# Performance work log

Measured on AMD Instinct MI355X. Metric: run time of the kernel, lower is better.

Reference implementation:

```python
import jax, jax.numpy as jnp
import numpy as np


def setup_inputs() -> dict:
    key = jax.random.key(0)
    ks = jax.random.split(key, 6)
    n_sess, n_trials = 4096, 2048
    chose_left = jax.random.bernoulli(ks[0], 0.5, (n_sess, n_trials)).astype(jnp.float32)
    chose_right = 1.0 - chose_left
    outcome = jax.random.bernoulli(ks[1], 0.5, (n_sess, n_trials)).astype(jnp.float32)
    inp = jnp.stack([chose_left, chose_right, outcome], axis=-1)  # (B, T, 3)
    return {
        "input": inp,
        # raw (pre-sigmoid) alpha logits, as stored by torch parametrize
        "a_same_rew": jax.random.normal(ks[2], (1,), jnp.float32),
        "a_same_unrew": jax.random.normal(ks[3], (1,), jnp.float32),
        "a_diff_rew": jax.random.normal(ks[4], (1,), jnp.float32),
        "a_diff_unrew": jax.random.normal(ks[5], (1,), jnp.float32),
        "k_same_rew": jnp.ones((1,), jnp.float32),
        "k_same_unrew": jnp.zeros((1,), jnp.float32),
        "k_diff_rew": jnp.ones((1,), jnp.float32),
        "k_diff_unrew": jnp.zeros((1,), jnp.float32),
    }


def _qvalue_scan(inp, a_sr, a_su, a_dr, a_du, k_sr, k_su, k_dr, k_du):
    # alphas via UnitConstraint (sigmoid of raw logit)
    alphas = jax.nn.sigmoid(jnp.concatenate([a_sr, a_su, a_dr, a_du]))  # (4,)
    ksr, ksu, kdr, kdu = k_sr[0], k_su[0], k_dr[0], k_du[0]
    B = inp.shape[0]

    def step(v, x_t):  # v: (B,2), x_t: (B,3)
        cl, cr, o = x_t[:, 0], x_t[:, 1], x_t[:, 2]
        no = 1.0 - o

        def side(same, other, vcol):
            d = jnp.stack([same * o * (ksr - vcol),
                           same * no * (ksu - vcol),
                           other * o * (kdr - vcol),
                           other * no * (kdu - vcol)], axis=1)  # (B,4)
            return d.sum(axis=1), d @ alphas  # diff, delta per side

        diff_l, del_l = side(cl, cr, v[:, 0])
        diff_r, del_r = side(cr, cl, v[:, 1])
        delta = jnp.stack([del_l, del_r], axis=1)  # (B,2)
        diff = jnp.stack([diff_l, diff_r], axis=1)
        new_v = v + delta
        return new_v, (new_v, diff, delta)

    v0 = jnp.zeros((B, 2), inp.dtype)
    _, (out_v, out_diff, out_delta) = jax.lax.scan(step, v0, jnp.swapaxes(inp, 0, 1))
    # (T,B,2) -> (B,T,2)
    tr = lambda a: jnp.swapaxes(a, 0, 1)
    return tr(out_v), tr(out_diff), tr(out_delta)


def reference(input, a_same_rew, a_same_unrew, a_diff_rew, a_diff_unrew,
              k_same_rew, k_same_unrew, k_diff_rew, k_diff_unrew):
    return _qvalue_scan(input, a_same_rew, a_same_unrew, a_diff_rew, a_diff_unrew,
                        k_same_rew, k_same_unrew, k_diff_rew, k_diff_unrew)
```

## Files before the change

kernel.cpp:

```cpp
#include <hip/hip_runtime.h>
#include <math.h>

#define B_SESS 4096
#define T_TR   2048
#define NCH    256
#define CL     8


__global__ __launch_bounds__(256, 4) void qvalue_kernel(
    const float* __restrict__ inp,
    const float* __restrict__ p_asr, const float* __restrict__ p_asu,
    const float* __restrict__ p_adr, const float* __restrict__ p_adu,
    const float* __restrict__ p_ksr, const float* __restrict__ p_ksu,
    const float* __restrict__ p_kdr, const float* __restrict__ p_kdu,
    float* __restrict__ out)
{
    __shared__ float sIn[T_TR * 3];
    __shared__ float sWT[4 * 4];

    const int s    = blockIdx.x;
    const int tid  = threadIdx.x;
    const int lane = tid & 63;
    const int w    = tid >> 6;

    const float4* in4 = (const float4*)(inp + (size_t)s * (T_TR * 3));
    #pragma unroll
    for (int k = 0; k < 6; ++k) {
        int p4 = k * 256 + tid;
        float4 wv = in4[p4];
        float vals[4] = {wv.x, wv.y, wv.z, wv.w};
        #pragma unroll
        for (int e = 0; e < 4; ++e) {
            int p = p4 * 4 + e;
            int t = p / 3;
            int c = p - t * 3;
            sIn[((t & (CL - 1)) * NCH + (t >> 3)) * 3 + c] = vals[e];
        }
    }

    float a0 = 1.f / (1.f + expf(-p_asr[0]));
    float a1 = 1.f / (1.f + expf(-p_asu[0]));
    float a2 = 1.f / (1.f + expf(-p_adr[0]));
    float a3 = 1.f / (1.f + expf(-p_adu[0]));
    float k0 = p_ksr[0], k1 = p_ksu[0], k2 = p_kdr[0], k3 = p_kdu[0];
    float b0 = a0 * k0, b1 = a1 * k1, b2 = a2 * k2, b3 = a3 * k3;

    __syncthreads();

    float AL = 1.f, BL = 0.f, AR = 1.f, BR = 0.f;
    #pragma unroll
    for (int l = 0; l < CL; ++l) {
        int base = (l * NCH + tid) * 3;
        float cl = sIn[base], cr = sIn[base + 1], o = sIn[base + 2];
        float no = 1.f - o;
        float m0 = cl * o, m1 = cl * no, m2 = cr * o, m3 = cr * no;
        float coefL = a0 * m0 + a1 * m1 + a2 * m2 + a3 * m3;
        float rhsL  = b0 * m0 + b1 * m1 + b2 * m2 + b3 * m3;
        float coefR = a0 * m2 + a1 * m3 + a2 * m0 + a3 * m1;
        float rhsR  = b0 * m2 + b1 * m3 + b2 * m0 + b3 * m1;
        float gL = 1.f - coefL, gR = 1.f - coefR;
        AL = AL * gL;  BL = BL * gL + rhsL;
        AR = AR * gR;  BR = BR * gR + rhsR;
    }

    #pragma unroll
    for (int d = 1; d < 64; d <<= 1) {
        float tAL = __shfl_up(AL, d, 64);
        float tBL = __shfl_up(BL, d, 64);
        float tAR = __shfl_up(AR, d, 64);
        float tBR = __shfl_up(BR, d, 64);
        if (lane >= d) {
            BL = AL * tBL + BL;  AL = AL * tAL;
            BR = AR * tBR + BR;  AR = AR * tAR;
        }
    }
    if (lane == 63) {
        sWT[w * 4 + 0] = AL;  sWT[w * 4 + 1] = BL;
        sWT[w * 4 + 2] = AR;  sWT[w * 4 + 3] = BR;
    }
    float eAL = __shfl_up(AL, 1, 64), eBL = __shfl_up(BL, 1, 64);
    float eAR = __shfl_up(AR, 1, 64), eBR = __shfl_up(BR, 1, 64);
    if (lane == 0) { eAL = 1.f; eBL = 0.f; eAR = 1.f; eBR = 0.f; }

    __syncthreads();

    float vbL = 0.f, vbR = 0.f;
    for (int ww = 0; ww < w; ++ww) {
        vbL = sWT[ww * 4 + 0] * vbL + sWT[ww * 4 + 1];
        vbR = sWT[ww * 4 + 2] * vbR + sWT[ww * 4 + 3];
    }
    float vL = eAL * vbL + eBL;
    float vR = eAR * vbR + eBR;

    float vb[2 * CL], fb[2 * CL], db[2 * CL];
    #pragma unroll
    for (int l = 0; l < CL; ++l) {
        int base = (l * NCH + tid) * 3;
        float cl = sIn[base], cr = sIn[base + 1], o = sIn[base + 2];
        float no = 1.f - o;
        float m0 = cl * o, m1 = cl * no, m2 = cr * o, m3 = cr * no;
        float coefL = a0 * m0 + a1 * m1 + a2 * m2 + a3 * m3;
        float rhsL  = b0 * m0 + b1 * m1 + b2 * m2 + b3 * m3;
        float coefR = a0 * m2 + a1 * m3 + a2 * m0 + a3 * m1;
        float rhsR  = b0 * m2 + b1 * m3 + b2 * m0 + b3 * m1;
        float s0  = m0 + m1 + m2 + m3;
        float s1L = k0 * m0 + k1 * m1 + k2 * m2 + k3 * m3;
        float s1R = k0 * m2 + k1 * m3 + k2 * m0 + k3 * m1;
        float dL = rhsL - coefL * vL;
        float dR = rhsR - coefR * vR;
        float fL = s1L - s0 * vL;
        float fR = s1R - s0 * vR;
        vL += dL;  vR += dR;
        vb[2 * l] = vL;  vb[2 * l + 1] = vR;
        fb[2 * l] = fL;  fb[2 * l + 1] = fR;
        db[2 * l] = dL;  db[2 * l + 1] = dR;
    }

    __syncthreads();
    float* rb = sIn + (w << 10);
    const size_t N2    = (size_t)B_SESS * T_TR * 2;
    const size_t gbase = (size_t)s * (T_TR * 2) + ((size_t)w << 10);

    float4* ov = (float4*)(out + gbase);
    float4* of = (float4*)(out + N2 + gbase);
    float4* od = (float4*)(out + 2 * N2 + gbase);

    #pragma unroll
    for (int q = 0; q < 4; ++q)
        ((float4*)(rb + lane * 16))[q] =
            make_float4(vb[4 * q], vb[4 * q + 1], vb[4 * q + 2], vb[4 * q + 3]);
    __syncthreads();
    #pragma unroll
    for (int q = 0; q < 4; ++q)
        ov[q * 64 + lane] = ((const float4*)rb)[q * 64 + lane];
    __syncthreads();

    #pragma unroll
    for (int q = 0; q < 4; ++q)
        ((float4*)(rb + lane * 16))[q] =
            make_float4(fb[4 * q], fb[4 * q + 1], fb[4 * q + 2], fb[4 * q + 3]);
    __syncthreads();
    #pragma unroll
    for (int q = 0; q < 4; ++q)
        of[q * 64 + lane] = ((const float4*)rb)[q * 64 + lane];
    __syncthreads();

    #pragma unroll
    for (int q = 0; q < 4; ++q)
        ((float4*)(rb + lane * 16))[q] =
            make_float4(db[4 * q], db[4 * q + 1], db[4 * q + 2], db[4 * q + 3]);
    __syncthreads();
    #pragma unroll
    for (int q = 0; q < 4; ++q)
        od[q * 64 + lane] = ((const float4*)rb)[q * 64 + lane];
}

extern "C" void kernel_launch(void* const* d_in, const int* in_sizes, int n_in,
                              void* d_out, int out_size, void* d_ws, size_t ws_size,
                              hipStream_t stream) {
    (void)in_sizes; (void)n_in; (void)out_size; (void)d_ws; (void)ws_size;
    qvalue_kernel<<<B_SESS, 256, 0, stream>>>(
        (const float*)d_in[0],
        (const float*)d_in[1], (const float*)d_in[2],
        (const float*)d_in[3], (const float*)d_in[4],
        (const float*)d_in[5], (const float*)d_in[6],
        (const float*)d_in[7], (const float*)d_in[8],
        (float*)d_out);
}
```

Measured before the change: 296.8 us.

## Use 512-thread blocks with contiguous per-thread chunks, dropping LDS staging

Each session is now handled by 512 threads, each owning 4 consecutive trials loaded directly from global memory as three float4 values. This removes the shared-memory transpose of inputs and the LDS-staged output writes along with their barriers. Outputs are written as float4 straight from registers. The cost is a wider cross-wave combine over 8 waves, and per-thread 32-byte store strides that are less perfectly coalesced than the staged version.

```diff
diff --git a/kernel.cpp b/kernel.cpp
--- a/kernel.cpp
+++ b/kernel.cpp
@@ -3,11 +3,11 @@
 
 #define B_SESS 4096
 #define T_TR   2048
-#define NCH    256
-#define CL     8
+#define BLK    512
+#define CLT    4
 
 
-__global__ __launch_bounds__(256, 4) void qvalue_kernel(
+__global__ __launch_bounds__(BLK, 8) void qvalue_kernel(
     const float* __restrict__ inp,
     const float* __restrict__ p_asr, const float* __restrict__ p_asu,
     const float* __restrict__ p_adr, const float* __restrict__ p_adu,
@@ -15,28 +15,18 @@
     const float* __restrict__ p_kdr, const float* __restrict__ p_kdu,
     float* __restrict__ out)
 {
-    __shared__ float sIn[T_TR * 3];
-    __shared__ float sWT[4 * 4];
+    __shared__ float sWT[8 * 4];
 
     const int s    = blockIdx.x;
     const int tid  = threadIdx.x;
     const int lane = tid & 63;
     const int w    = tid >> 6;
 
-    const float4* in4 = (const float4*)(inp + (size_t)s * (T_TR * 3));
-    #pragma unroll
-    for (int k = 0; k < 6; ++k) {
-        int p4 = k * 256 + tid;
-        float4 wv = in4[p4];
-        float vals[4] = {wv.x, wv.y, wv.z, wv.w};
-        #pragma unroll
-        for (int e = 0; e < 4; ++e) {
-            int p = p4 * 4 + e;
-            int t = p / 3;
-            int c = p - t * 3;
-            sIn[((t & (CL - 1)) * NCH + (t >> 3)) * 3 + c] = vals[e];
-        }
-    }
+    const float4* in4 = (const float4*)(inp + (size_t)s * (T_TR * 3)) + tid * 3;
+    float4 x0 = in4[0], x1 = in4[1], x2 = in4[2];
+    float cl[CLT] = {x0.x, x0.w, x1.z, x2.y};
+    float cr[CLT] = {x0.y, x1.x, x1.w, x2.z};
+    float oo[CLT] = {x0.z, x1.y, x2.x, x2.w};
 
     float a0 = 1.f / (1.f + expf(-p_asr[0]));
     float a1 = 1.f / (1.f + expf(-p_asu[0]));
@@ -45,22 +35,18 @@
     float k0 = p_ksr[0], k1 = p_ksu[0], k2 = p_kdr[0], k3 = p_kdu[0];
     float b0 = a0 * k0, b1 = a1 * k1, b2 = a2 * k2, b3 = a3 * k3;
 
-    __syncthreads();
-
     float AL = 1.f, BL = 0.f, AR = 1.f, BR = 0.f;
     #pragma unroll
-    for (int l = 0; l < CL; ++l) {
-        int base = (l * NCH + tid) * 3;
-        float cl = sIn[base], cr = sIn[base + 1], o = sIn[base + 2];
-        float no = 1.f - o;
-        float m0 = cl * o, m1 = cl * no, m2 = cr * o, m3 = cr * no;
+    for (int i = 0; i < CLT; ++i) {
+        float o = oo[i], no = 1.f - o;
+        float m0 = cl[i] * o, m1 = cl[i] * no, m2 = cr[i] * o, m3 = cr[i] * no;
         float coefL = a0 * m0 + a1 * m1 + a2 * m2 + a3 * m3;
         float rhsL  = b0 * m0 + b1 * m1 + b2 * m2 + b3 * m3;
         float coefR = a0 * m2 + a1 * m3 + a2 * m0 + a3 * m1;
         float rhsR  = b0 * m2 + b1 * m3 + b2 * m0 + b3 * m1;
         float gL = 1.f - coefL, gR = 1.f - coefR;
-        AL = AL * gL;  BL = BL * gL + rhsL;
-        AR = AR * gR;  BR = BR * gR + rhsR;
+        AL = gL * AL;  BL = gL * BL + rhsL;
+        AR = gR * AR;  BR = gR * BR + rhsR;
     }
 
     #pragma unroll
@@ -92,74 +78,45 @@
     float vL = eAL * vbL + eBL;
     float vR = eAR * vbR + eBR;
 
-    float vb[2 * CL], fb[2 * CL], db[2 * CL];
-    #pragma unroll
-    for (int l = 0; l < CL; ++l) {
-        int base = (l * NCH + tid) * 3;
-        float cl = sIn[base], cr = sIn[base + 1], o = sIn[base + 2];
-        float no = 1.f - o;
-        float m0 = cl * o, m1 = cl * no, m2 = cr * o, m3 = cr * no;
-        float coefL = a0 * m0 + a1 * m1 + a2 * m2 + a3 * m3;
-        float rhsL  = b0 * m0 + b1 * m1 + b2 * m2 + b3 * m3;
-        float coefR = a0 * m2 + a1 * m3 + a2 * m0 + a3 * m1;
-        float rhsR  = b0 * m2 + b1 * m3 + b2 * m0 + b3 * m1;
-        float s0  = m0 + m1 + m2 + m3;
-        float s1L = k0 * m0 + k1 * m1 + k2 * m2 + k3 * m3;
-        float s1R = k0 * m2 + k1 * m3 + k2 * m0 + k3 * m1;
-        float dL = rhsL - coefL * vL;
-        float dR = rhsR - coefR * vR;
-        float fL = s1L - s0 * vL;
-        float fR = s1R - s0 * vR;
-        vL += dL;  vR += dR;
-        vb[2 * l] = vL;  vb[2 * l + 1] = vR;
-        fb[2 * l] = fL;  fb[2 * l + 1] = fR;
-        db[2 * l] = dL;  db[2 * l + 1] = dR;
-    }
-
-    __syncthreads();
-    float* rb = sIn + (w << 10);
-    const size_t N2    = (size_t)B_SESS * T_TR * 2;
-    const size_t gbase = (size_t)s * (T_TR * 2) + ((size_t)w << 10);
-
-    float4* ov = (float4*)(out + gbase);
-    float4* of = (float4*)(out + N2 + gbase);
-    float4* od = (float4*)(out + 2 * N2 + gbase);
+    const size_t N2 = (size_t)B_SESS * T_TR * 2;
+    float4* ov = (float4*)(out)          + (size_t)s * 1024 + tid * 2;
+    float4* of = (float4*)(out + N2)     + (size_t)s * 1024 + tid * 2;
+    float4* od = (float4*)(out + 2 * N2) + (size_t)s * 1024 + tid * 2;
 
     #pragma unroll
-    for (int q = 0; q < 4; ++q)
-        ((float4*)(rb + lane * 16))[q] =
-            make_float4(vb[4 * q], vb[4 * q + 1], vb[4 * q + 2], vb[4 * q + 3]);
-    __syncthreads();
-    #pragma unroll
-    for (int q = 0; q < 4; ++q)
-        ov[q * 64 + lane] = ((const float4*)rb)[q * 64 + lane];
-    __syncthreads();
-
-    #pragma unroll
-    for (int q = 0; q < 4; ++q)
-        ((float4*)(rb + lane * 16))[q] =
-            make_float4(fb[4 * q], fb[4 * q + 1], fb[4 * q + 2], fb[4 * q + 3]);
-    __syncthreads();
-    #pragma unroll
-    for (int q = 0; q < 4; ++q)
-        of[q * 64 + lane] = ((const float4*)rb)[q * 64 + lane];
-    __syncthreads();
-
-    #pragma unroll
-    for (int q = 0; q < 4; ++q)
-        ((float4*)(rb + lane * 16))[q] =
-            make_float4(db[4 * q], db[4 * q + 1], db[4 * q + 2], db[4 * q + 3]);
-    __syncthreads();
-    #pragma unroll
-    for (int q = 0; q < 4; ++q)
-        od[q * 64 + lane] = ((const float4*)rb)[q * 64 + lane];
+    for (int p = 0; p < 2; ++p) {
+        float v4[4], f4[4], d4[4];
+        #pragma unroll
+        for (int j = 0; j < 2; ++j) {
+            int i = 2 * p + j;
+            float o = oo[i], no = 1.f - o;
+            float m0 = cl[i] * o, m1 = cl[i] * no, m2 = cr[i] * o, m3 = cr[i] * no;
+            float coefL = a0 * m0 + a1 * m1 + a2 * m2 + a3 * m3;
+            float rhsL  = b0 * m0 + b1 * m1 + b2 * m2 + b3 * m3;
+            float coefR = a0 * m2 + a1 * m3 + a2 * m0 + a3 * m1;
+            float rhsR  = b0 * m2 + b1 * m3 + b2 * m0 + b3 * m1;
+            float s0  = m0 + m1 + m2 + m3;
+            float s1L = k0 * m0 + k1 * m1 + k2 * m2 + k3 * m3;
+            float s1R = k0 * m2 + k1 * m3 + k2 * m0 + k3 * m1;
+            float dL = rhsL - coefL * vL;
+            float dR = rhsR - coefR * vR;
+            f4[2 * j]     = s1L - s0 * vL;
+            f4[2 * j + 1] = s1R - s0 * vR;
+            vL += dL;  vR += dR;
+            v4[2 * j] = vL;  v4[2 * j + 1] = vR;
+            d4[2 * j] = dL;  d4[2 * j + 1] = dR;
+        }
+        ov[p] = make_float4(v4[0], v4[1], v4[2], v4[3]);
+        of[p] = make_float4(f4[0], f4[1], f4[2], f4[3]);
+        od[p] = make_float4(d4[0], d4[1], d4[2], d4[3]);
+    }
 }
 
 extern "C" void kernel_launch(void* const* d_in, const int* in_sizes, int n_in,
                               void* d_out, int out_size, void* d_ws, size_t ws_size,
                               hipStream_t stream) {
     (void)in_sizes; (void)n_in; (void)out_size; (void)d_ws; (void)ws_size;
-    qvalue_kernel<<<B_SESS, 256, 0, stream>>>(
+    qvalue_kernel<<<B_SESS, BLK, 0, stream>>>(
         (const float*)d_in[0],
         (const float*)d_in[1], (const float*)d_in[2],
         (const float*)d_in[3], (const float*)d_in[4],
```

Result: no change. 299.7 us (+1.0%).
